# Kernel tuning notes

Hardware: AMD Instinct MI355X
Metric: run time of the kernel (lower is better)

The kernel has to match this reference:

```python
import jax, jax.numpy as jnp
import numpy as np

B = 16       # graphs per batch
N = 256      # nodes per graph (Hi-C submatrix bins)
NT = B * N   # total nodes
E = 131072   # total edges
DIN = 32     # input feature dim (HYPERPARAMETERS['input_shape'])
H1, H2 = 16, 32
HID = 32     # ContactCNN hidden dim
W7 = 7       # final conv width


def setup_inputs() -> dict:
    key = jax.random.key(0)
    ks = jax.random.split(key, 16)
    x = jax.random.normal(ks[0], (NT, DIN), dtype=jnp.float32)
    edge_index = jax.random.randint(ks[1], (2, E), 0, NT, dtype=jnp.int64)
    edge_attr = jax.random.uniform(ks[2], (E,), dtype=jnp.float32)
    batch_index = jnp.repeat(jnp.arange(B, dtype=jnp.int64), N)
    s = 0.1
    params = dict(
        W0=jax.random.normal(ks[3], (DIN, H1), dtype=jnp.float32) * s,
        b0=jnp.zeros((H1,), dtype=jnp.float32),
        W1=jax.random.normal(ks[4], (H1, H2), dtype=jnp.float32) * s,
        b1=jnp.zeros((H2,), dtype=jnp.float32),
        W2=jax.random.normal(ks[5], (H2, H2), dtype=jnp.float32) * s,
        b2=jnp.zeros((H2,), dtype=jnp.float32),
        Wc=jax.random.normal(ks[6], (HID, H2), dtype=jnp.float32) * s,  # 1x1 conv: [out=HID, in=H2]
        bc=jnp.zeros((HID,), dtype=jnp.float32),
        Wp=jax.random.normal(ks[7], (1, HID, W7, W7), dtype=jnp.float32) * s,  # OIHW
        bp=jnp.zeros((1,), dtype=jnp.float32),
    )
    return dict(x=x, edge_index=edge_index, edge_attr=edge_attr,
                batch_index=batch_index, **params)


def _gcn_norm(edge_index, edge_weight, n):
    # PyG gcn_norm with improved=True (self-loop fill value 2.0)
    src, dst = edge_index[0], edge_index[1]
    loop = jnp.arange(n, dtype=src.dtype)
    src_a = jnp.concatenate([src, loop])
    dst_a = jnp.concatenate([dst, loop])
    w_a = jnp.concatenate([edge_weight, jnp.full((n,), 2.0, dtype=edge_weight.dtype)])
    deg = jax.ops.segment_sum(w_a, dst_a, num_segments=n)
    deg_safe = jnp.where(deg > 0, deg, 1.0)
    dinv = jnp.where(deg > 0, jax.lax.rsqrt(deg_safe), 0.0)
    norm = dinv[src_a] * w_a * dinv[dst_a]
    return src_a, dst_a, norm


def _gcn_layer(h, W, b, src_a, dst_a, norm, n):
    h = h @ W                                  # [n, out]
    msg = norm[:, None] * h[src_a]             # gather + scale
    return jax.ops.segment_sum(msg, dst_a, num_segments=n) + b  # scatter-add


def reference(x, edge_index, edge_attr, batch_index,
              W0, b0, W1, b1, W2, b2, Wc, bc, Wp, bp):
    n = x.shape[0]
    src_a, dst_a, norm = _gcn_norm(edge_index, edge_attr, n)
    h = jax.nn.relu(_gcn_layer(x, W0, b0, src_a, dst_a, norm, n))
    h = jax.nn.relu(_gcn_layer(h, W1, b1, src_a, dst_a, norm, n))
    h = jax.nn.relu(_gcn_layer(h, W2, b2, src_a, dst_a, norm, n))
    z = h.reshape(B, N, -1)                    # process_graph_batch
    # ContactCNN: broadcast outer product -> 1x1 conv -> ReLU -> 7x7 conv -> sigmoid
    zm = jnp.einsum('bid,bjd->bdij', z, z)     # [B, D, N, N]
    c = jax.nn.relu(jnp.einsum('bdij,hd->bhij', zm, Wc) + bc[None, :, None, None])
    s = jax.lax.conv_general_dilated(
        c, Wp, window_strides=(1, 1), padding='SAME',
        dimension_numbers=('NCHW', 'OIHW', 'NCHW')) + bp[None, :, None, None]
    return jax.nn.sigmoid(s)                   # [B, 1, N, N]
```

## Files before the change

### kernel.cpp

```cpp
#include <hip/hip_runtime.h>
#include <hip/hip_bf16.h>
#include <hip/hip_fp16.h>

#define NT 4096
#define NE 131072

#define OFF_DEG  0
#define OFF_A    16384
#define OFF_G1T  33570816
#define OFF_G2T  33701888
#define OFF_G3T  33964032
#define OFF_C    16384
#define OFF_H3   67125248
#define OFF_W2T  67387392

typedef __attribute__((ext_vector_type(8))) short bf16x8;
typedef __attribute__((ext_vector_type(4))) float f32x4;

__device__ inline unsigned int align16(unsigned int hi, unsigned int lo) {
#if __has_builtin(__builtin_amdgcn_alignbit)
    return __builtin_amdgcn_alignbit(hi, lo, 16);
#else
    return (lo >> 16) | (hi << 16);
#endif
}

__device__ inline unsigned short bfb(float x) {
    return __hip_bfloat16_raw(__float2bfloat16(x)).x;
}

__device__ inline void atomic_add_bf16(unsigned short* base, unsigned int idx, float v) {
    unsigned long long addr = (unsigned long long)(base + (idx & ~1u));
    unsigned int bits = ((unsigned int)bfb(v)) << ((idx & 1u) * 16);
    asm volatile("global_atomic_pk_add_bf16 %0, %1, off" :: "v"(addr), "v"(bits) : "memory");
}


__global__ void k_deg(const int* __restrict__ ei, const float* __restrict__ ew,
                      float* __restrict__ deg) {
    int e = blockIdx.x * 256 + threadIdx.x;
    if (e < NE) atomicAdd(&deg[ei[NE + e]], ew[e]);
}

__global__ void k_scatter(const int* __restrict__ ei, const float* __restrict__ ew,
                          const float* __restrict__ deg, unsigned short* __restrict__ A16,
                          const float* __restrict__ x, const float* __restrict__ W0,
                          unsigned short* __restrict__ G1T,
                          const float* __restrict__ Wp, unsigned int* __restrict__ w2) {
    int e = blockIdx.x * 256 + threadIdx.x;
    if (e < NE) {
        int s = ei[e], d = ei[NE + e];
        float v = rsqrtf(deg[s] + 2.f) * ew[e] * rsqrtf(deg[d] + 2.f);
        atomic_add_bf16(A16, (unsigned int)d * 4096u + (unsigned int)s, v);
    }
    if (e < NT) {
        atomic_add_bf16(A16, (unsigned int)e * 4097u, 2.f / (deg[e] + 2.f));
    }
    if (e < NT * 16) {
        int node = e & 4095, co = e >> 12;
        const float4* xr = (const float4*)(x + node * 32);
        float a = 0.f;
        #pragma unroll
        for (int r = 0; r < 8; r++) {
            float4 f = xr[r];
            a += f.x * W0[(r*4+0)*16 + co] + f.y * W0[(r*4+1)*16 + co]
               + f.z * W0[(r*4+2)*16 + co] + f.w * W0[(r*4+3)*16 + co];
        }
        G1T[co * 4096 + node] = bfb(a);
    }
    if (e >= NE - 1568) {
        int k = e - (NE - 1568);
        __half hh = __float2half(Wp[k]);
        __half2 h2 = __halves2half2(hh, hh);
        w2[k] = *(unsigned int*)&h2;
    }
}


template <int NIN, int NOUT, bool LAST>
__global__ __launch_bounds__(512) void k_gcn(const unsigned short* __restrict__ A16,
                                             const unsigned short* __restrict__ Gt,
                                             const float* __restrict__ bias,
                                             const float* __restrict__ W,
                                             unsigned short* __restrict__ Gout) {
    constexpr int T = NIN / 16;
    __shared__ float red[8][T][16][16];
    __shared__ unsigned short wtile[16 * 40];
    int mt = blockIdx.x;
    int tid = threadIdx.x;
    int w = tid >> 6, lane = tid & 63, m = lane & 15, q = lane >> 4;
    int kw = w * 512;

    const unsigned short* arow = A16 + (size_t)(mt * 16 + m) * 4096 + kw + q * 8;
    f32x4 acc[T];
    #pragma unroll
    for (int t = 0; t < T; t++) acc[t] = (f32x4){0.f, 0.f, 0.f, 0.f};

    bf16x8 wfrag;
    if (!LAST && w < NOUT / 16) {
        #pragma unroll
        for (int j = 0; j < 8; j++) {
            int ci = q * 8 + j;
            wfrag[j] = (ci < NIN) ? (short)bfb(W[ci * NOUT + w * 16 + m]) : (short)0;
        }
    }

    #pragma unroll 4
    for (int s = 0; s < 16; s++) {
        bf16x8 bA = *(const bf16x8*)(arow + s * 32);
        #pragma unroll
        for (int t = 0; t < T; t++) {
            bf16x8 af = *(const bf16x8*)(Gt + (size_t)(t * 16 + m) * 4096 + kw + q * 8 + s * 32);
            acc[t] = __builtin_amdgcn_mfma_f32_16x16x32_bf16(af, bA, acc[t], 0, 0, 0);
        }
    }
    #pragma unroll
    for (int t = 0; t < T; t++)
        #pragma unroll
        for (int r = 0; r < 4; r++) red[w][t][q*4 + r][m] = acc[t][r];
    __syncthreads();

    if (tid < T * 256) {
        int dstp = tid & 15, cop = (tid >> 4) & 15, t = tid >> 8;
        float sum = 0.f;
        #pragma unroll
        for (int w8 = 0; w8 < 8; w8++) sum += red[w8][t][cop][dstp];
        int co = t * 16 + cop;
        float val = fmaxf(sum + bias[co], 0.f);
        if (LAST) Gout[(size_t)(mt * 16 + dstp) * 32 + co] = bfb(val);
        else      wtile[dstp * 40 + co] = bfb(val);
    }
    if (!LAST && NIN == 16 && tid >= 256 && tid < 512) {
        int idx = tid - 256;
        wtile[(idx & 15) * 40 + 16 + ((idx >> 4) & 15)] = 0;
    }
    __syncthreads();

    if (!LAST && w < NOUT / 16) {
        bf16x8 af = *(const bf16x8*)&wtile[m * 40 + q * 8];
        f32x4 o = (f32x4){0.f, 0.f, 0.f, 0.f};
        o = __builtin_amdgcn_mfma_f32_16x16x32_bf16(af, wfrag, o, 0, 0, 0);
        uint2 ov;
        ov.x = (unsigned int)bfb(o[0]) | ((unsigned int)bfb(o[1]) << 16);
        ov.y = (unsigned int)bfb(o[2]) | ((unsigned int)bfb(o[3]) << 16);
        *(uint2*)&Gout[(size_t)(w * 16 + m) * 4096 + mt * 16 + q * 4] = ov;
    }
}


__global__ __launch_bounds__(256) void k_c1(const unsigned short* __restrict__ h3,
                                            const float* __restrict__ Wc,
                                            const float* __restrict__ bc,
                                            unsigned short* __restrict__ c) {
    __shared__ unsigned short zb[256 * 40];
    __shared__ unsigned short zwb[256 * 40];
    int blk = blockIdx.x;
    int b = blk >> 5, h = blk & 31;
    int tid = threadIdx.x;
    int lane = tid & 63, w = tid >> 6;
    int m = lane & 15, q = lane >> 4;

    {
        const uint4* zp = (const uint4*)(h3 + (size_t)(b * 256 + tid) * 32);
        unsigned int zr[16];
        #pragma unroll
        for (int k = 0; k < 4; k++) ((uint4*)zr)[k] = zp[k];
        unsigned int uw[16];
        #pragma unroll
        for (int k = 0; k < 16; k++) {
            float lo = __uint_as_float(zr[k] << 16);
            float hi = __uint_as_float(zr[k] & 0xffff0000u);
            float wl = Wc[h * 32 + 2 * k];
            float wh = Wc[h * 32 + 2 * k + 1];
            uw[k] = (unsigned int)bfb(lo * wl) | ((unsigned int)bfb(hi * wh) << 16);
        }
        uint4* zbp = (uint4*)&zb[tid * 40];
        uint4* zwp = (uint4*)&zwb[tid * 40];
        #pragma unroll
        for (int k = 0; k < 4; k++) {
            zbp[k] = ((uint4*)zr)[k];
            zwp[k] = ((uint4*)uw)[k];
        }
    }
    __syncthreads();

    bf16x8 bt[16];
    #pragma unroll
    for (int nt = 0; nt < 16; nt++)
        bt[nt] = *(const bf16x8*)&zb[(nt * 16 + m) * 40 + q * 8];

    bf16x8 af[4];
    #pragma unroll
    for (int s = 0; s < 4; s++)
        af[s] = *(const bf16x8*)&zwb[((w * 4 + s) * 16 + m) * 40 + q * 8];

    float bch = bc[h];
    size_t plane = ((size_t)blk) << 16;

    #pragma unroll
    for (int s = 0; s < 4; s++) {
        f32x4 acc[16];
        #pragma unroll
        for (int nt = 0; nt < 16; nt++) {
            acc[nt] = (f32x4){0.f, 0.f, 0.f, 0.f};
            acc[nt] = __builtin_amdgcn_mfma_f32_16x16x32_bf16(af[s], bt[nt], acc[nt], 0, 0, 0);
        }
        int jbase = (w * 4 + s) * 16 + q * 4;
        #pragma unroll
        for (int nt = 0; nt < 16; nt++) {
            float v0 = fmaxf(acc[nt][0] + bch, 0.f);
            float v1 = fmaxf(acc[nt][1] + bch, 0.f);
            float v2 = fmaxf(acc[nt][2] + bch, 0.f);
            float v3 = fmaxf(acc[nt][3] + bch, 0.f);
            __half2 p0 = __floats2half2_rn(v0, v1);
            __half2 p1 = __floats2half2_rn(v2, v3);
            uint2 o;
            o.x = *(unsigned int*)&p0;
            o.y = *(unsigned int*)&p1;
            *(uint2*)&c[plane + (size_t)(nt * 16 + m) * 256 + jbase] = o;
        }
    }
}


__global__ __launch_bounds__(256) void k_conv(const __half* __restrict__ c,
                                              const unsigned int* __restrict__ w2,
                                              const float* __restrict__ bp,
                                              float* __restrict__ out) {
    __shared__ __align__(16) unsigned int tile[2][70 * 38];
    int b = blockIdx.z, i0 = blockIdx.y * 64, j0 = blockIdx.x * 64;
    int tid = threadIdx.x;
    int tx = tid & 15, ty = tid >> 4;

    int goff[11]; int loff[11]; bool gok[11]; bool sok[11];
    #pragma unroll
    for (int k = 0; k < 11; k++) {
        int idx = tid + k * 256;
        sok[k] = idx < 2590;
        int r = idx / 37, cc = idx - r * 37;
        int gi = i0 - 3 + r;
        int gdw = (j0 >> 1) - 2 + cc;
        gok[k] = sok[k] && gi >= 0 && gi < 256 && gdw >= 0 && gdw < 128;
        goff[k] = gok[k] ? (gi * 128 + gdw) : 0;
        loff[k] = r * 38 + cc;
    }

    const unsigned int* cgd = (const unsigned int*)c;
    {
        const unsigned int* cp = cgd + ((size_t)(b * 32) << 15);
        #pragma unroll
        for (int k = 0; k < 11; k++) {
            unsigned int v = gok[k] ? cp[goff[k]] : 0u;
            if (sok[k]) tile[0][loff[k]] = v;
        }
    }
    __syncthreads();

    __half2 acc[4][2];
    __half2 z2 = __float2half2_rn(0.f);
    #pragma unroll
    for (int o = 0; o < 4; o++) { acc[o][0] = z2; acc[o][1] = z2; }

    for (int h = 0; h < 32; h++) {
        unsigned int sv[11];
        if (h < 31) {
            const unsigned int* cp = cgd + ((size_t)(b * 32 + h + 1) << 15);
            #pragma unroll
            for (int k = 0; k < 11; k++) sv[k] = gok[k] ? cp[goff[k]] : 0u;
        }

        const unsigned int* T = &tile[h & 1][0];
        const __half2* wrow = (const __half2*)w2 + h * 49;
        #pragma unroll
        for (int r8 = 0; r8 < 10; r8++) {
            const unsigned int* rp = T + (ty * 4 + r8) * 38 + tx * 2;
            uint2 ea = *(const uint2*)rp;
            uint2 eb = *(const uint2*)(rp + 2);
            uint2 ec = *(const uint2*)(rp + 4);
            unsigned int E[6] = {ea.x, ea.y, eb.x, eb.y, ec.x, ec.y};
            unsigned int O[5];
            #pragma unroll
            for (int k = 0; k < 5; k++) O[k] = align16(E[k + 1], E[k]);
            #pragma unroll
            for (int o = 0; o < 4; o++) {
                int di = r8 - o;
                if (di < 0 || di > 6) continue;
                #pragma unroll
                for (int dj = 0; dj < 7; dj++) {
                    __half2 wv = wrow[di * 7 + dj];
                    int d = dj - 3;
                    unsigned int p0 = (d & 1) ? O[(d + 3) >> 1] : E[(d + 4) >> 1];
                    unsigned int p1 = (d & 1) ? O[((d + 3) >> 1) + 1] : E[((d + 4) >> 1) + 1];
                    acc[o][0] = __hfma2(wv, *(__half2*)&p0, acc[o][0]);
                    acc[o][1] = __hfma2(wv, *(__half2*)&p1, acc[o][1]);
                }
            }
        }

        if (h < 31) {
            unsigned int* Tn = &tile[(h + 1) & 1][0];
            #pragma unroll
            for (int k = 0; k < 11; k++) if (sok[k]) Tn[loff[k]] = sv[k];
        }
        __syncthreads();
    }

    float bpv = bp[0];
    #pragma unroll
    for (int o = 0; o < 4; o++) {
        float2 f0 = __half22float2(acc[o][0]);
        float2 f1 = __half22float2(acc[o][1]);
        float4 r;
        r.x = 1.0f / (1.0f + __expf(-(f0.x + bpv)));
        r.y = 1.0f / (1.0f + __expf(-(f0.y + bpv)));
        r.z = 1.0f / (1.0f + __expf(-(f1.x + bpv)));
        r.w = 1.0f / (1.0f + __expf(-(f1.y + bpv)));
        *(float4*)&out[((size_t)(b * 256 + i0 + ty * 4 + o)) * 256 + j0 + tx * 4] = r;
    }
}


extern "C" void kernel_launch(void* const* d_in, const int* in_sizes, int n_in,
                              void* d_out, int out_size, void* d_ws, size_t ws_size,
                              hipStream_t stream) {
    const float* x  = (const float*)d_in[0];
    const int*   ei = (const int*)d_in[1];
    const float* ew = (const float*)d_in[2];
    const float* W0 = (const float*)d_in[4];
    const float* b0 = (const float*)d_in[5];
    const float* W1 = (const float*)d_in[6];
    const float* b1 = (const float*)d_in[7];
    const float* W2 = (const float*)d_in[8];
    const float* b2 = (const float*)d_in[9];
    const float* Wc = (const float*)d_in[10];
    const float* bc = (const float*)d_in[11];
    const float* Wp = (const float*)d_in[12];
    const float* bp = (const float*)d_in[13];

    char* ws = (char*)d_ws;
    float*          deg  = (float*)(ws + OFF_DEG);
    unsigned short* A16  = (unsigned short*)(ws + OFF_A);
    unsigned short* G1T  = (unsigned short*)(ws + OFF_G1T);
    unsigned short* G2T  = (unsigned short*)(ws + OFF_G2T);
    unsigned short* G3T  = (unsigned short*)(ws + OFF_G3T);
    unsigned short* H3   = (unsigned short*)(ws + OFF_H3);
    unsigned int*   w2t  = (unsigned int*)(ws + OFF_W2T);
    unsigned short* cbuf = (unsigned short*)(ws + OFF_C);

    (void)hipMemsetAsync(d_ws, 0, 16384 + 33554432, stream);

    k_deg    <<<NE/256, 256, 0, stream>>>(ei, ew, deg);
    k_scatter<<<NE/256, 256, 0, stream>>>(ei, ew, deg, A16, x, W0, G1T, Wp, w2t);

    k_gcn<16, 32, false><<<256, 512, 0, stream>>>(A16, G1T, b0, W1, G2T);
    k_gcn<32, 32, false><<<256, 512, 0, stream>>>(A16, G2T, b1, W2, G3T);
    k_gcn<32, 32, true> <<<256, 512, 0, stream>>>(A16, G3T, b2, nullptr, H3);

    k_c1  <<<512, 256, 0, stream>>>(H3, Wc, bc, cbuf);
    k_conv<<<dim3(4,4,16), 256, 0, stream>>>((const __half*)cbuf, w2t, bp, (float*)d_out);
}
```

Measured before the change: 237.3 us.

## Fuse 1x1 contact conv into 7x7 conv kernel, keeping C planes in LDS

```diff
diff --git a/kernel.cpp b/kernel.cpp
--- a/kernel.cpp
+++ b/kernel.cpp
@@ -10,9 +10,8 @@
 #define OFF_G1T  33570816
 #define OFF_G2T  33701888
 #define OFF_G3T  33964032
-#define OFF_C    16384
-#define OFF_H3   67125248
-#define OFF_W2T  67387392
+#define OFF_H3   34226176
+#define OFF_W2T  34488320
 
 typedef __attribute__((ext_vector_type(8))) short bf16x8;
 typedef __attribute__((ext_vector_type(4))) float f32x4;
@@ -148,174 +147,161 @@
 }
 
 
-__global__ __launch_bounds__(256) void k_c1(const unsigned short* __restrict__ h3,
+__global__ __launch_bounds__(512) void k_cc(const unsigned short* __restrict__ h3,
                                             const float* __restrict__ Wc,
                                             const float* __restrict__ bc,
-                                            unsigned short* __restrict__ c) {
-    __shared__ unsigned short zb[256 * 40];
-    __shared__ unsigned short zwb[256 * 40];
-    int blk = blockIdx.x;
-    int b = blk >> 5, h = blk & 31;
+                                            const unsigned int* __restrict__ w2,
+                                            const float* __restrict__ bp,
+                                            float* __restrict__ out) {
+    __shared__ unsigned short zs[256 * 40];
+    __shared__ float wcs[32 * 36];
+    __shared__ __align__(16) unsigned short ct[4 * 32 * 272];
+    __shared__ __align__(16) unsigned short pt[4][4096];
+
+    int band = blockIdx.x, bb = blockIdx.y;
+    int i0 = band * 16;
     int tid = threadIdx.x;
     int lane = tid & 63, w = tid >> 6;
     int m = lane & 15, q = lane >> 4;
 
     {
-        const uint4* zp = (const uint4*)(h3 + (size_t)(b * 256 + tid) * 32);
-        unsigned int zr[16];
-        #pragma unroll
-        for (int k = 0; k < 4; k++) ((uint4*)zr)[k] = zp[k];
-        unsigned int uw[16];
-        #pragma unroll
-        for (int k = 0; k < 16; k++) {
-            float lo = __uint_as_float(zr[k] << 16);
-            float hi = __uint_as_float(zr[k] & 0xffff0000u);
-            float wl = Wc[h * 32 + 2 * k];
-            float wh = Wc[h * 32 + 2 * k + 1];
-            uw[k] = (unsigned int)bfb(lo * wl) | ((unsigned int)bfb(hi * wh) << 16);
-        }
-        uint4* zbp = (uint4*)&zb[tid * 40];
-        uint4* zwp = (uint4*)&zwb[tid * 40];
-        #pragma unroll
-        for (int k = 0; k < 4; k++) {
-            zbp[k] = ((uint4*)zr)[k];
-            zwp[k] = ((uint4*)uw)[k];
-        }
-    }
+        int row = tid >> 1, half = tid & 1;
+        const uint4* src = (const uint4*)(h3 + (size_t)(bb * 256 + row) * 32) + half * 2;
+        uint4 v0 = src[0], v1 = src[1];
+        uint4* dst = (uint4*)&zs[row * 40 + half * 16];
+        dst[0] = v0; dst[1] = v1;
+    }
+    #pragma unroll
+    for (int k = tid; k < 1024; k += 512) wcs[(k >> 5) * 36 + (k & 31)] = Wc[k];
+    for (int k = tid; k < 4 * 32 * 136; k += 512) ((unsigned int*)ct)[k] = 0;
     __syncthreads();
 
-    bf16x8 bt[16];
-    #pragma unroll
-    for (int nt = 0; nt < 16; nt++)
-        bt[nt] = *(const bf16x8*)&zb[(nt * 16 + m) * 40 + q * 8];
-
-    bf16x8 af[4];
-    #pragma unroll
-    for (int s = 0; s < 4; s++)
-        af[s] = *(const bf16x8*)&zwb[((w * 4 + s) * 16 + m) * 40 + q * 8];
-
-    float bch = bc[h];
-    size_t plane = ((size_t)blk) << 16;
-
-    #pragma unroll
-    for (int s = 0; s < 4; s++) {
-        f32x4 acc[16];
-        #pragma unroll
-        for (int nt = 0; nt < 16; nt++) {
-            acc[nt] = (f32x4){0.f, 0.f, 0.f, 0.f};
-            acc[nt] = __builtin_amdgcn_mfma_f32_16x16x32_bf16(af[s], bt[nt], acc[nt], 0, 0, 0);
-        }
-        int jbase = (w * 4 + s) * 16 + q * 4;
-        #pragma unroll
-        for (int nt = 0; nt < 16; nt++) {
-            float v0 = fmaxf(acc[nt][0] + bch, 0.f);
-            float v1 = fmaxf(acc[nt][1] + bch, 0.f);
-            float v2 = fmaxf(acc[nt][2] + bch, 0.f);
-            float v3 = fmaxf(acc[nt][3] + bch, 0.f);
-            __half2 p0 = __floats2half2_rn(v0, v1);
-            __half2 p1 = __floats2half2_rn(v2, v3);
-            uint2 o;
-            o.x = *(unsigned int*)&p0;
-            o.y = *(unsigned int*)&p1;
-            *(uint2*)&c[plane + (size_t)(nt * 16 + m) * 256 + jbase] = o;
-        }
-    }
-}
-
-
-__global__ __launch_bounds__(256) void k_conv(const __half* __restrict__ c,
-                                              const unsigned int* __restrict__ w2,
-                                              const float* __restrict__ bp,
-                                              float* __restrict__ out) {
-    __shared__ __align__(16) unsigned int tile[2][70 * 38];
-    int b = blockIdx.z, i0 = blockIdx.y * 64, j0 = blockIdx.x * 64;
-    int tid = threadIdx.x;
-    int tx = tid & 15, ty = tid >> 4;
-
-    int goff[11]; int loff[11]; bool gok[11]; bool sok[11];
-    #pragma unroll
-    for (int k = 0; k < 11; k++) {
-        int idx = tid + k * 256;
-        sok[k] = idx < 2590;
-        int r = idx / 37, cc = idx - r * 37;
-        int gi = i0 - 3 + r;
-        int gdw = (j0 >> 1) - 2 + cc;
-        gok[k] = sok[k] && gi >= 0 && gi < 256 && gdw >= 0 && gdw < 128;
-        goff[k] = gok[k] ? (gi * 128 + gdw) : 0;
-        loff[k] = r * 38 + cc;
-    }
-
-    const unsigned int* cgd = (const unsigned int*)c;
-    {
-        const unsigned int* cp = cgd + ((size_t)(b * 32) << 15);
-        #pragma unroll
-        for (int k = 0; k < 11; k++) {
-            unsigned int v = gok[k] ? cp[goff[k]] : 0u;
-            if (sok[k]) tile[0][loff[k]] = v;
-        }
-    }
-    __syncthreads();
-
-    __half2 acc[4][2];
-    __half2 z2 = __float2half2_rn(0.f);
-    #pragma unroll
-    for (int o = 0; o < 4; o++) { acc[o][0] = z2; acc[o][1] = z2; }
-
-    for (int h = 0; h < 32; h++) {
-        unsigned int sv[11];
-        if (h < 31) {
-            const unsigned int* cp = cgd + ((size_t)(b * 32 + h + 1) << 15);
+    bf16x8 bt[2];
+    bool wok[2];
+    #pragma unroll
+    for (int nt = 0; nt < 2; nt++) {
+        int r = i0 - 3 + nt * 16 + m;
+        wok[nt] = (unsigned)r < 256u;
+        r = r < 0 ? 0 : (r > 255 ? 255 : r);
+        bt[nt] = *(const bf16x8*)&zs[r * 40 + q * 8];
+    }
+    float zaf[2][8];
+    #pragma unroll
+    for (int jt2 = 0; jt2 < 2; jt2++) {
+        bf16x8 za = *(const bf16x8*)&zs[((w * 2 + jt2) * 16 + m) * 40 + q * 8];
+        #pragma unroll
+        for (int e = 0; e < 8; e++)
+            zaf[jt2][e] = __uint_as_float(((unsigned int)(unsigned short)za[e]) << 16);
+    }
+
+    int gg = tid >> 7, tx = tid & 31, ty = (tid >> 5) & 3;
+    __half2 acc[4][4];
+    __half2 zh = __float2half2_rn(0.f);
+    #pragma unroll
+    for (int o = 0; o < 4; o++)
+        #pragma unroll
+        for (int p = 0; p < 4; p++) acc[o][p] = zh;
+
+    for (int it = 0; it < 8; it++) {
+        #pragma unroll
+        for (int g = 0; g < 4; g++) {
+            int h = it * 4 + g;
+            float wf[8];
+            *(float4*)&wf[0] = *(const float4*)&wcs[h * 36 + q * 8];
+            *(float4*)&wf[4] = *(const float4*)&wcs[h * 36 + q * 8 + 4];
+            float bch = bc[h];
             #pragma unroll
-            for (int k = 0; k < 11; k++) sv[k] = gok[k] ? cp[goff[k]] : 0u;
-        }
-
-        const unsigned int* T = &tile[h & 1][0];
-        const __half2* wrow = (const __half2*)w2 + h * 49;
-        #pragma unroll
-        for (int r8 = 0; r8 < 10; r8++) {
-            const unsigned int* rp = T + (ty * 4 + r8) * 38 + tx * 2;
-            uint2 ea = *(const uint2*)rp;
-            uint2 eb = *(const uint2*)(rp + 2);
-            uint2 ec = *(const uint2*)(rp + 4);
-            unsigned int E[6] = {ea.x, ea.y, eb.x, eb.y, ec.x, ec.y};
-            unsigned int O[5];
-            #pragma unroll
-            for (int k = 0; k < 5; k++) O[k] = align16(E[k + 1], E[k]);
-            #pragma unroll
-            for (int o = 0; o < 4; o++) {
-                int di = r8 - o;
-                if (di < 0 || di > 6) continue;
+            for (int jt2 = 0; jt2 < 2; jt2++) {
+                bf16x8 afv;
                 #pragma unroll
-                for (int dj = 0; dj < 7; dj++) {
-                    __half2 wv = wrow[di * 7 + dj];
-                    int d = dj - 3;
-                    unsigned int p0 = (d & 1) ? O[(d + 3) >> 1] : E[(d + 4) >> 1];
-                    unsigned int p1 = (d & 1) ? O[((d + 3) >> 1) + 1] : E[((d + 4) >> 1) + 1];
-                    acc[o][0] = __hfma2(wv, *(__half2*)&p0, acc[o][0]);
-                    acc[o][1] = __hfma2(wv, *(__half2*)&p1, acc[o][1]);
+                for (int e = 0; e < 8; e++) afv[e] = (short)bfb(zaf[jt2][e] * wf[e]);
+                int pos = 4 + (w * 2 + jt2) * 16 + q * 4;
+                #pragma unroll
+                for (int nt = 0; nt < 2; nt++) {
+                    f32x4 d = (f32x4){0.f, 0.f, 0.f, 0.f};
+                    d = __builtin_amdgcn_mfma_f32_16x16x32_bf16(afv, bt[nt], d, 0, 0, 0);
+                    if (wok[nt]) {
+                        float v0 = fmaxf(d[0] + bch, 0.f);
+                        float v1 = fmaxf(d[1] + bch, 0.f);
+                        float v2 = fmaxf(d[2] + bch, 0.f);
+                        float v3 = fmaxf(d[3] + bch, 0.f);
+                        __half2 h0 = __floats2half2_rn(v0, v1);
+                        __half2 h1 = __floats2half2_rn(v2, v3);
+                        uint2 o2;
+                        o2.x = *(unsigned int*)&h0;
+                        o2.y = *(unsigned int*)&h1;
+                        *(uint2*)&ct[g * 8704 + (nt * 16 + m) * 272 + pos] = o2;
+                    }
                 }
             }
         }
-
-        if (h < 31) {
-            unsigned int* Tn = &tile[(h + 1) & 1][0];
+        __syncthreads();
+
+        {
+            const unsigned short* C = ct + gg * 8704;
+            const __half2* wrow = (const __half2*)w2 + (it * 4 + gg) * 49;
             #pragma unroll
-            for (int k = 0; k < 11; k++) if (sok[k]) Tn[loff[k]] = sv[k];
+            for (int dr = 0; dr < 10; dr++) {
+                const uint4* p4 = (const uint4*)&C[(ty * 4 + dr) * 272 + tx * 8];
+                uint4 ua = p4[0], ub = p4[1];
+                unsigned int E[8] = {ua.x, ua.y, ua.z, ua.w, ub.x, ub.y, ub.z, ub.w};
+                unsigned int O[7];
+                #pragma unroll
+                for (int k = 0; k < 7; k++) O[k] = align16(E[k + 1], E[k]);
+                #pragma unroll
+                for (int o = 0; o < 4; o++) {
+                    if (dr - o < 0 || dr - o > 6) continue;
+                    int di = dr - o;
+                    #pragma unroll
+                    for (int dj = 0; dj < 7; dj++) {
+                        __half2 wv = wrow[di * 7 + dj];
+                        #pragma unroll
+                        for (int pr = 0; pr < 4; pr++) {
+                            int s = 2 * pr + dj + 1;
+                            unsigned int pv = (s & 1) ? O[s >> 1] : E[s >> 1];
+                            acc[o][pr] = __hfma2(wv, *(__half2*)&pv, acc[o][pr]);
+                        }
+                    }
+                }
+            }
         }
         __syncthreads();
     }
 
-    float bpv = bp[0];
     #pragma unroll
     for (int o = 0; o < 4; o++) {
-        float2 f0 = __half22float2(acc[o][0]);
-        float2 f1 = __half22float2(acc[o][1]);
-        float4 r;
-        r.x = 1.0f / (1.0f + __expf(-(f0.x + bpv)));
-        r.y = 1.0f / (1.0f + __expf(-(f0.y + bpv)));
-        r.z = 1.0f / (1.0f + __expf(-(f1.x + bpv)));
-        r.w = 1.0f / (1.0f + __expf(-(f1.y + bpv)));
-        *(float4*)&out[((size_t)(b * 256 + i0 + ty * 4 + o)) * 256 + j0 + tx * 4] = r;
+        uint4 v;
+        v.x = *(unsigned int*)&acc[o][0];
+        v.y = *(unsigned int*)&acc[o][1];
+        v.z = *(unsigned int*)&acc[o][2];
+        v.w = *(unsigned int*)&acc[o][3];
+        *(uint4*)&pt[gg][(ty * 4 + o) * 256 + tx * 8] = v;
+    }
+    __syncthreads();
+
+    {
+        int base = tid * 8;
+        float fs[8];
+        #pragma unroll
+        for (int e = 0; e < 8; e++) fs[e] = 0.f;
+        #pragma unroll
+        for (int g = 0; g < 4; g++) {
+            uint4 v = *(const uint4*)&pt[g][base];
+            unsigned int uu[4] = {v.x, v.y, v.z, v.w};
+            #pragma unroll
+            for (int d = 0; d < 4; d++) {
+                float2 f = __half22float2(*(__half2*)&uu[d]);
+                fs[2 * d] += f.x; fs[2 * d + 1] += f.y;
+            }
+        }
+        float bpv = bp[0];
+        float rs[8];
+        #pragma unroll
+        for (int e = 0; e < 8; e++) rs[e] = 1.0f / (1.0f + __expf(-(fs[e] + bpv)));
+        int row = base >> 8, col = base & 255;
+        float* op = &out[((size_t)(bb * 256) + i0 + row) * 256 + col];
+        *(float4*)op = make_float4(rs[0], rs[1], rs[2], rs[3]);
+        *(float4*)(op + 4) = make_float4(rs[4], rs[5], rs[6], rs[7]);
     }
 }
 
@@ -345,7 +331,6 @@
     unsigned short* G3T  = (unsigned short*)(ws + OFF_G3T);
     unsigned short* H3   = (unsigned short*)(ws + OFF_H3);
     unsigned int*   w2t  = (unsigned int*)(ws + OFF_W2T);
-    unsigned short* cbuf = (unsigned short*)(ws + OFF_C);
 
     (void)hipMemsetAsync(d_ws, 0, 16384 + 33554432, stream);
 
@@ -356,6 +341,5 @@
     k_gcn<32, 32, false><<<256, 512, 0, stream>>>(A16, G2T, b1, W2, G3T);
     k_gcn<32, 32, true> <<<256, 512, 0, stream>>>(A16, G3T, b2, nullptr, H3);
 
-    k_c1  <<<512, 256, 0, stream>>>(H3, Wc, bc, cbuf);
-    k_conv<<<dim3(4,4,16), 256, 0, stream>>>((const __half*)cbuf, w2t, bp, (float*)d_out);
-}
+    k_cc<<<dim3(16, 16), 512, 0, stream>>>(H3, Wc, bc, w2t, bp, (float*)d_out);
+}
```

Result: faster. 196.5 us (-17.2%).
